# Kernel optimization log

Measured on AMD Instinct MI355X. Metric: run time of the kernel, lower is better.

## Reference

```python
import jax, jax.numpy as jnp
import numpy as np

VAR0, VAR1 = 0.1, 0.2          # SSD encode variances
POS_T, NEG_T, NPR = 0.5, 0.4, 3  # pos/neg thresholds, negpos_ratio
BBOX_ALPHA, CONF_ALPHA = 1.5, 1.0


def point_form(b):
    # cxcywh -> x1y1x2y2
    return jnp.concatenate([b[..., :2] - b[..., 2:] / 2, b[..., :2] + b[..., 2:] / 2], -1)


def jaccard(a, b):
    # a:[n,4], b:[m,4] in xyxy -> IoU [n,m]
    tl = jnp.maximum(a[:, None, :2], b[None, :, :2])
    br = jnp.minimum(a[:, None, 2:], b[None, :, 2:])
    inter = jnp.prod(jnp.clip(br - tl, 0.0), -1)
    area_a = jnp.prod(a[:, 2:] - a[:, :2], -1)[:, None]
    area_b = jnp.prod(b[:, 2:] - b[:, :2], -1)[None, :]
    return inter / jnp.clip(area_a + area_b - inter, 1e-10)


def encode(matched, priors):
    # matched: xyxy GT per prior; priors: cxcywh
    g_c = ((matched[:, :2] + matched[:, 2:]) / 2 - priors[:, :2]) / (VAR0 * priors[:, 2:])
    g_wh = jnp.log(jnp.clip((matched[:, 2:] - matched[:, :2]) / priors[:, 2:], 1e-8)) / VAR1
    return jnp.concatenate([g_c, g_wh], -1)


def match_one(gt_box, gt_lab, priors):
    # gt_box:[G,4] xyxy, gt_lab:[G], priors:[P,4] cxcywh
    ov = jaccard(gt_box, point_form(priors))            # [G,P]
    bt_over = ov.max(0)                                  # best GT overlap per prior [P]
    bt_idx = ov.argmax(0)                                # [P]
    bp_idx = ov.argmax(1)                                # best prior per GT [G]
    G = gt_box.shape[0]
    bt_over = bt_over.at[bp_idx].set(2.0)                # force-match best priors
    bt_idx = bt_idx.at[bp_idx].set(jnp.arange(G))
    matched = gt_box[bt_idx]                             # [P,4]
    conf_t = gt_lab[bt_idx]
    conf_t = jnp.where(bt_over < POS_T, jnp.where(bt_over < NEG_T, 0, -1), conf_t)
    return encode(matched, priors), conf_t


def reference(loc_data, conf_data, priors, gt_bboxes, gt_labels):
    B, P, C = conf_data.shape
    loc_t, conf_t = jax.vmap(match_one)(gt_bboxes, gt_labels, priors)
    loc_t = jax.lax.stop_gradient(loc_t)                 # targets are detached in torch
    pos = conf_t > 0                                     # [B,P]
    num_pos = pos.sum(-1)                                # [B]
    dt = loc_data.dtype
    pos_w = pos.astype(dt) / jnp.clip(num_pos, 1).astype(dt)[:, None]

    # localization: per-image-normalized smooth L1 over positives
    d = loc_data - loc_t
    sl1 = jnp.where(jnp.abs(d) < 1.0, 0.5 * d * d, jnp.abs(d) - 0.5)
    loss_B = (pos_w[:, :, None] * sl1).sum() * BBOX_ALPHA

    # OHEM confidence loss: mine top negpos_ratio*num_pos hardest negatives per image
    loss_c = jax.nn.logsumexp(conf_data, -1) - conf_data[..., 0]
    loss_c = jnp.where(pos | (conf_t < 0), 0.0, jax.lax.stop_gradient(loss_c))
    rank = jnp.argsort(jnp.argsort(-loss_c, -1), -1)     # descending rank [B,P]
    num_neg = jnp.clip(NPR * num_pos, 0, P - 1)
    neg = (rank < num_neg[:, None]) & (conf_t == 0)
    keep = (pos | neg).astype(dt)
    logp = jax.nn.log_softmax(conf_data, -1)
    tgt = jnp.clip(conf_t, 0)
    ce = -jnp.take_along_axis(logp, tgt[..., None], -1)[..., 0]
    loss_C = (keep * ce).sum() * CONF_ALPHA

    return jnp.stack([loss_B, loss_C]) / B               # [2]: (loss_B, loss_C)


def setup_inputs() -> dict:
    key = jax.random.key(0)
    k = jax.random.split(key, 8)
    B, P, C, G = 16, 19248, 81, 16
    loc_data = jax.random.normal(k[0], (B, P, 4), jnp.float32)
    conf_data = jax.random.normal(k[1], (B, P, C), jnp.float32)
    pc = jax.random.uniform(k[2], (B, P, 2)) * 0.9 + 0.05
    pwh = jax.random.uniform(k[3], (B, P, 2)) * 0.25 + 0.05
    priors = jnp.concatenate([pc, pwh], -1).astype(jnp.float32)  # cxcywh
    gc = jax.random.uniform(k[4], (B, G, 2)) * 0.8 + 0.1
    gwh = jax.random.uniform(k[5], (B, G, 2)) * 0.3 + 0.05
    gt_bboxes = jnp.clip(point_form(jnp.concatenate([gc, gwh], -1)), 0.0, 1.0).astype(jnp.float32)
    gt_labels = jax.random.randint(k[6], (B, G), 1, C)
    return {"loc_data": loc_data, "conf_data": conf_data, "priors": priors,
            "gt_bboxes": gt_bboxes, "gt_labels": gt_labels}
```

## Files before the change

### kernel.cpp

```cpp
#include <hip/hip_runtime.h>
#include <math.h>

#define NB 16
#define NP 19248
#define NC 81
#define NG 16
#define NBLK 76
#define NBC 301
#define NWPB (NBC * 4)

static __device__ __forceinline__ float smoothl1(float d) {
    float a = fabsf(d);
    return (a < 1.f) ? 0.5f * d * d : (a - 0.5f);
}

static __device__ __forceinline__ unsigned long long umax64(unsigned long long a, unsigned long long b) {
    return a > b ? a : b;
}

__global__ void k_init(unsigned int* w, float* out) {
    if (threadIdx.x < 512) w[threadIdx.x] = 0u;
    if (threadIdx.x < 2) out[threadIdx.x] = 0.f;
}

__global__ void k_match(const float* __restrict__ priors,
                        const float* __restrict__ gtb,
                        float* __restrict__ bt_over, int* __restrict__ bt_idx,
                        unsigned long long* __restrict__ bp_key) {
    const int b = blockIdx.y;
    const int p = blockIdx.x * 256 + threadIdx.x;
    const bool valid = p < NP;
    __shared__ float4 sgt[NG];
    __shared__ unsigned long long smax[NG];
    if (threadIdx.x < NG) {
        const float* g4 = gtb + (size_t)(b * NG + threadIdx.x) * 4;
        sgt[threadIdx.x] = make_float4(g4[0], g4[1], g4[2], g4[3]);
        smax[threadIdx.x] = 0ULL;
    }
    __syncthreads();
    float4 pr = make_float4(0.f, 0.f, 0.f, 0.f);
    if (valid) pr = *(const float4*)(priors + ((size_t)b * NP + p) * 4);
    float px1 = pr.x - pr.z * 0.5f, py1 = pr.y - pr.w * 0.5f;
    float px2 = pr.x + pr.z * 0.5f, py2 = pr.y + pr.w * 0.5f;
    float areaP = (px2 - px1) * (py2 - py1);
    float best = -1.f; int bi = 0;
    unsigned int pk = 0xFFFFFFFFu - (unsigned int)p;
    #pragma unroll
    for (int g = 0; g < NG; ++g) {
        float4 gb = sgt[g];
        float iw = fminf(gb.z, px2) - fmaxf(gb.x, px1);
        float ih = fminf(gb.w, py2) - fmaxf(gb.y, py1);
        float inter = fmaxf(iw, 0.f) * fmaxf(ih, 0.f);
        float areaG = (gb.z - gb.x) * (gb.w - gb.y);
        float ov = inter / fmaxf(areaG + areaP - inter, 1e-10f);
        if (ov > best) { best = ov; bi = g; }
        unsigned long long key = ((unsigned long long)__float_as_uint(ov) << 32) | pk;
        #pragma unroll
        for (int off = 1; off <= 8; off <<= 1)
            key = umax64(key, (unsigned long long)__shfl_xor((unsigned long long)key, off));
        if ((threadIdx.x & 15) == 0) atomicMax(&smax[g], key);
    }
    if (valid) {
        bt_over[(size_t)b * NP + p] = best;
        bt_idx[(size_t)b * NP + p] = bi;
    }
    __syncthreads();
    if (threadIdx.x < NG) atomicMax(&bp_key[b * NG + threadIdx.x], smax[threadIdx.x]);
}

__global__ void __launch_bounds__(256, 6) k_conf(
        const float* __restrict__ conf,
        const float* __restrict__ loc,
        const float* __restrict__ priors,
        const float* __restrict__ gtb,
        const int* __restrict__ gtl,
        const float* __restrict__ bt_over,
        const int* __restrict__ bt_idx,
        const unsigned long long* __restrict__ bp_key,
        float* __restrict__ mlc,
        int* __restrict__ pnp, float* __restrict__ psl, float* __restrict__ pce) {
    __shared__ float sc[4][1296];
    const int b = blockIdx.y;
    const int tid = threadIdx.x;
    const int w = tid >> 6, lane = tid & 63;
    const int rb = blockIdx.x * 64 + w * 16;
    const bool wvalid = rb < NP;
    const int rb_c = wvalid ? rb : (NP - 16);

    const float4* src = (const float4*)(conf + ((size_t)b * NP + rb_c) * 81);
    float4* dst = (float4*)sc[w];
    #pragma unroll
    for (int i = 0; i < 5; ++i) dst[lane + 64 * i] = src[lane + 64 * i];
    if (lane < 4) dst[lane + 320] = src[lane + 320];
    __builtin_amdgcn_wave_barrier();

    const int r = lane >> 2, c = lane & 3;
    const int p = rb_c + r;
    const int bp = b * NP + p;

    const float over = bt_over[bp];
    int bi = bt_idx[bp];
    int ct;
    if (over < 0.4f) ct = 0;
    else if (over < 0.5f) ct = -1;
    else ct = gtl[b * NG + bi];
    #pragma unroll
    for (int g = NG - 1; g >= 0; --g) {
        unsigned int fp = 0xFFFFFFFFu - (unsigned int)(bp_key[b * NG + g] & 0xFFFFFFFFULL);
        if (fp == (unsigned int)p) { bi = g; ct = gtl[b * NG + g]; break; }
    }
    if (!wvalid) ct = 0;
    const int tgt = ct > 0 ? ct : 0;

    const float* row = sc[w] + r * 81;
    float s = 0.f, ctg = 0.f;
    #pragma unroll
    for (int k = 0; k < 21; ++k) {
        int cc = c + 4 * k;
        if (cc < 81) {
            float v = row[cc];
            s += __expf(v);
            ctg += (cc == tgt) ? v : 0.f;
        }
    }
    s += __shfl_xor(s, 1, 4);   s += __shfl_xor(s, 2, 4);
    ctg += __shfl_xor(ctg, 1, 4); ctg += __shfl_xor(ctg, 2, 4);
    const float c0 = row[0];
    const float lse = __logf(s);

    if (c == 0 && wvalid) mlc[bp] = (ct == 0) ? (lse - c0) : -1.0f;

    float vsl = 0.f, vce = 0.f; int vnp = 0;
    if (c == 0 && ct > 0) {
        const float4 prr = *(const float4*)(priors + (size_t)bp * 4);
        const float* gb = gtb + (size_t)(b * NG + bi) * 4;
        float lt0 = ((gb[0] + gb[2]) * 0.5f - prr.x) / (0.1f * prr.z);
        float lt1 = ((gb[1] + gb[3]) * 0.5f - prr.y) / (0.1f * prr.w);
        float lt2 = logf(fmaxf((gb[2] - gb[0]) / prr.z, 1e-8f)) / 0.2f;
        float lt3 = logf(fmaxf((gb[3] - gb[1]) / prr.w, 1e-8f)) / 0.2f;
        const float4 l4 = *(const float4*)(loc + (size_t)bp * 4);
        vsl = smoothl1(l4.x - lt0) + smoothl1(l4.y - lt1) +
              smoothl1(l4.z - lt2) + smoothl1(l4.w - lt3);
        vce = lse - ctg;
        vnp = 1;
    }
    #pragma unroll
    for (int o = 32; o >= 1; o >>= 1) {
        vnp += __shfl_xor(vnp, o);
        vsl += __shfl_xor(vsl, o);
        vce += __shfl_xor(vce, o);
    }
    if (lane == 0) {
        const int idx = b * NWPB + blockIdx.x * 4 + w;
        pnp[idx] = vnp; psl[idx] = vsl; pce[idx] = vce;
    }
}

__global__ void __launch_bounds__(1024) k_selneg(
        const float* __restrict__ mlc,
        const int* __restrict__ pnp,
        const float* __restrict__ psl,
        const float* __restrict__ pce,
        float* __restrict__ out) {
    const int b = blockIdx.x, tid = threadIdx.x;
    __shared__ unsigned int hist[4096];
    __shared__ unsigned long long list[1024];
    __shared__ unsigned int s_jstar, s_need, s_cnt;
    __shared__ unsigned long long s_thr;
    __shared__ unsigned int wtot[16], wsuf[16];
    __shared__ float wsum[16];
    __shared__ int wnp[16]; __shared__ float wsl[16], wcp[16];
    __shared__ int s_np; __shared__ float s_sl, s_cp;

    const float4* v4 = (const float4*)(mlc + (size_t)b * NP);
    float4 rv[5];
    #pragma unroll
    for (int j = 0; j < 5; ++j) {
        int i = tid + 1024 * j;
        rv[j] = (i < NP / 4) ? v4[i] : make_float4(-1.f, -1.f, -1.f, -1.f);
    }

    {
        int np_ = 0; float sl_ = 0.f, cp_ = 0.f;
        for (int i = tid; i < NWPB; i += 1024) {
            np_ += pnp[b * NWPB + i];
            sl_ += psl[b * NWPB + i];
            cp_ += pce[b * NWPB + i];
        }
        #pragma unroll
        for (int o = 32; o >= 1; o >>= 1) {
            np_ += __shfl_xor(np_, o);
            sl_ += __shfl_xor(sl_, o);
            cp_ += __shfl_xor(cp_, o);
        }
        if ((tid & 63) == 0) { wnp[tid >> 6] = np_; wsl[tid >> 6] = sl_; wcp[tid >> 6] = cp_; }
    }
    if (tid == 0) { s_cnt = 0u; s_thr = ~0ULL; }
    for (int i = tid; i < 4096; i += 1024) hist[i] = 0u;
    __syncthreads();
    if (tid == 0) {
        int np_ = 0; float sl_ = 0.f, cp_ = 0.f;
        #pragma unroll
        for (int i = 0; i < 16; ++i) { np_ += wnp[i]; sl_ += wsl[i]; cp_ += wcp[i]; }
        s_np = np_; s_sl = sl_; s_cp = cp_;
    }
    #pragma unroll
    for (int j = 0; j < 5; ++j) {
        float vv[4] = {rv[j].x, rv[j].y, rv[j].z, rv[j].w};
        #pragma unroll
        for (int c = 0; c < 4; ++c)
            if (vv[c] >= 0.f)
                atomicAdd(&hist[min((unsigned int)(vv[c] * 256.f), 4095u)], 1u);
    }
    __syncthreads();
    const int np = s_np;
    const unsigned int k = (unsigned int)min(3 * np, NP - 1);

    if (k > 0) {
        unsigned int c0 = hist[tid * 4], c1 = hist[tid * 4 + 1],
                     c2 = hist[tid * 4 + 2], c3 = hist[tid * 4 + 3];
        unsigned int t2 = c2 + c3, t1 = c1 + t2, t0 = c0 + t1;
        unsigned int s = t0;
        const int lane = tid & 63, w = tid >> 6;
        #pragma unroll
        for (int o = 1; o < 64; o <<= 1) {
            unsigned int vv = __shfl_down(s, o);
            if (lane + o < 64) s += vv;
        }
        if (lane == 0) wtot[w] = s;
        __syncthreads();
        if (tid < 16) {
            unsigned int acc = 0;
            for (int j = tid + 1; j < 16; ++j) acc += wtot[j];
            wsuf[tid] = acc;
        }
        __syncthreads();
        const unsigned int base = wsuf[w] + (s - t0);
        unsigned int b0 = base + t0, b1 = base + t1, b2 = base + t2, b3 = base + c3;
        hist[tid * 4] = b0; hist[tid * 4 + 1] = b1;
        hist[tid * 4 + 2] = b2; hist[tid * 4 + 3] = b3;
        __syncthreads();
        const unsigned int total = hist[0];
        if (k >= total) {
            if (tid == 0) s_thr = 0ULL;
        } else {
            unsigned int n3 = (tid * 4 + 4 < 4096) ? hist[tid * 4 + 4] : 0u;
            if (b0 >= k && b1 < k) { s_jstar = tid * 4;     s_need = k - b1; }
            if (b1 >= k && b2 < k) { s_jstar = tid * 4 + 1; s_need = k - b2; }
            if (b2 >= k && b3 < k) { s_jstar = tid * 4 + 2; s_need = k - b3; }
            if (b3 >= k && n3 < k) { s_jstar = tid * 4 + 3; s_need = k - n3; }
            __syncthreads();
            const unsigned int jstar = s_jstar, need = s_need;
            #pragma unroll
            for (int j = 0; j < 5; ++j) {
                float vv[4] = {rv[j].x, rv[j].y, rv[j].z, rv[j].w};
                #pragma unroll
                for (int c = 0; c < 4; ++c) {
                    if (vv[c] >= 0.f &&
                        min((unsigned int)(vv[c] * 256.f), 4095u) == jstar) {
                        unsigned int pos = atomicAdd(&s_cnt, 1u);
                        if (pos < 1024u) {
                            int pidx = 4 * (tid + 1024 * j) + c;
                            list[pos] = ((unsigned long long)__float_as_uint(vv[c]) << 32) |
                                        (unsigned long long)(0xFFFFFFFFu - (unsigned int)pidx);
                        }
                    }
                }
            }
            __syncthreads();
            const unsigned int cnt = s_cnt;
            if (cnt <= 1024u) {
                if (tid < (int)cnt) {
                    unsigned long long me = list[tid];
                    unsigned int rk = 0;
                    for (unsigned int j = 0; j < cnt; ++j) rk += (list[j] > me) ? 1u : 0u;
                    if (rk == need - 1) s_thr = me;
                }
            } else if (tid == 0) {
                s_thr = ((unsigned long long)__float_as_uint((float)jstar / 256.f)) << 32;
            }
        }
    }
    __syncthreads();
    const unsigned long long thr = s_thr;

    float sum = 0.f;
    #pragma unroll
    for (int j = 0; j < 5; ++j) {
        float vv[4] = {rv[j].x, rv[j].y, rv[j].z, rv[j].w};
        #pragma unroll
        for (int c = 0; c < 4; ++c) {
            if (vv[c] >= 0.f) {
                int pidx = 4 * (tid + 1024 * j) + c;
                unsigned long long key = ((unsigned long long)__float_as_uint(vv[c]) << 32) |
                                         (unsigned long long)(0xFFFFFFFFu - (unsigned int)pidx);
                if (key >= thr) sum += vv[c];
            }
        }
    }
    #pragma unroll
    for (int o = 32; o >= 1; o >>= 1) sum += __shfl_xor(sum, o);
    if ((tid & 63) == 0) wsum[tid >> 6] = sum;
    __syncthreads();
    if (tid == 0) {
        float neg = 0.f;
        #pragma unroll
        for (int i = 0; i < 16; ++i) neg += wsum[i];
        float lb = s_sl / (float)max(np, 1);
        float lc = s_cp + neg;
        atomicAdd(&out[0], lb * 1.5f / (float)NB);
        atomicAdd(&out[1], lc / (float)NB);
    }
}

extern "C" void kernel_launch(void* const* d_in, const int* in_sizes, int n_in,
                              void* d_out, int out_size, void* d_ws, size_t ws_size,
                              hipStream_t stream) {
    const float* loc    = (const float*)d_in[0];
    const float* conf   = (const float*)d_in[1];
    const float* priors = (const float*)d_in[2];
    const float* gtb    = (const float*)d_in[3];
    const int*   gtl    = (const int*)d_in[4];
    float* out = (float*)d_out;

    char* w = (char*)d_ws;
    const size_t BP4 = (size_t)NB * NP * 4;
    const size_t P1  = (size_t)NB * NWPB * 4;
    unsigned long long* bp_key = (unsigned long long*)w;
    int*   pnp = (int*)  (w + 4096);
    float* psl = (float*)(w + 4096 + P1);
    float* pce = (float*)(w + 4096 + 2 * P1);
    float* bt_over  = (float*)(w + 262144);
    int*   bt_idx   = (int*)  (w + 262144 + BP4);
    float* mlc      = (float*)(w + 262144 + 2 * BP4);

    k_init<<<1, 512, 0, stream>>>((unsigned int*)w, out);
    k_match<<<dim3(NBLK, NB), 256, 0, stream>>>(priors, gtb, bt_over, bt_idx, bp_key);
    k_conf<<<dim3(NBC, NB), 256, 0, stream>>>(conf, loc, priors, gtb, gtl,
                                              bt_over, bt_idx, bp_key, mlc,
                                              pnp, psl, pce);
    k_selneg<<<NB, 1024, 0, stream>>>(mlc, pnp, psl, pce, out);
}
```

Measured before the change: 188.0 us.

## Recompute per-prior best-GT overlap in conf kernel instead of storing it

```diff
diff --git a/kernel.cpp b/kernel.cpp
--- a/kernel.cpp
+++ b/kernel.cpp
@@ -5,7 +5,7 @@
 #define NP 19248
 #define NC 81
 #define NG 16
-#define NBLK 76
+#define NBM 19
 #define NBC 301
 #define NWPB (NBC * 4)
 
@@ -25,11 +25,8 @@
 
 __global__ void k_match(const float* __restrict__ priors,
                         const float* __restrict__ gtb,
-                        float* __restrict__ bt_over, int* __restrict__ bt_idx,
                         unsigned long long* __restrict__ bp_key) {
     const int b = blockIdx.y;
-    const int p = blockIdx.x * 256 + threadIdx.x;
-    const bool valid = p < NP;
     __shared__ float4 sgt[NG];
     __shared__ unsigned long long smax[NG];
     if (threadIdx.x < NG) {
@@ -38,44 +35,48 @@
         smax[threadIdx.x] = 0ULL;
     }
     __syncthreads();
-    float4 pr = make_float4(0.f, 0.f, 0.f, 0.f);
-    if (valid) pr = *(const float4*)(priors + ((size_t)b * NP + p) * 4);
-    float px1 = pr.x - pr.z * 0.5f, py1 = pr.y - pr.w * 0.5f;
-    float px2 = pr.x + pr.z * 0.5f, py2 = pr.y + pr.w * 0.5f;
-    float areaP = (px2 - px1) * (py2 - py1);
-    float best = -1.f; int bi = 0;
-    unsigned int pk = 0xFFFFFFFFu - (unsigned int)p;
+    unsigned long long kb[NG];
+    #pragma unroll
+    for (int g = 0; g < NG; ++g) kb[g] = 0ULL;
+    #pragma unroll
+    for (int i = 0; i < 4; ++i) {
+        const int p = blockIdx.x * 1024 + i * 256 + threadIdx.x;
+        const bool valid = p < NP;
+        float4 pr = make_float4(0.f, 0.f, 0.f, 0.f);
+        if (valid) pr = *(const float4*)(priors + ((size_t)b * NP + p) * 4);
+        float px1 = pr.x - pr.z * 0.5f, py1 = pr.y - pr.w * 0.5f;
+        float px2 = pr.x + pr.z * 0.5f, py2 = pr.y + pr.w * 0.5f;
+        float areaP = (px2 - px1) * (py2 - py1);
+        unsigned int pk = 0xFFFFFFFFu - (unsigned int)p;
+        #pragma unroll
+        for (int g = 0; g < NG; ++g) {
+            float4 gb = sgt[g];
+            float iw = fminf(gb.z, px2) - fmaxf(gb.x, px1);
+            float ih = fminf(gb.w, py2) - fmaxf(gb.y, py1);
+            float inter = fmaxf(iw, 0.f) * fmaxf(ih, 0.f);
+            float areaG = (gb.z - gb.x) * (gb.w - gb.y);
+            float ov = inter / fmaxf(areaG + areaP - inter, 1e-10f);
+            kb[g] = umax64(kb[g], ((unsigned long long)__float_as_uint(ov) << 32) | pk);
+        }
+    }
     #pragma unroll
     for (int g = 0; g < NG; ++g) {
-        float4 gb = sgt[g];
-        float iw = fminf(gb.z, px2) - fmaxf(gb.x, px1);
-        float ih = fminf(gb.w, py2) - fmaxf(gb.y, py1);
-        float inter = fmaxf(iw, 0.f) * fmaxf(ih, 0.f);
-        float areaG = (gb.z - gb.x) * (gb.w - gb.y);
-        float ov = inter / fmaxf(areaG + areaP - inter, 1e-10f);
-        if (ov > best) { best = ov; bi = g; }
-        unsigned long long key = ((unsigned long long)__float_as_uint(ov) << 32) | pk;
+        unsigned long long key = kb[g];
         #pragma unroll
         for (int off = 1; off <= 8; off <<= 1)
             key = umax64(key, (unsigned long long)__shfl_xor((unsigned long long)key, off));
         if ((threadIdx.x & 15) == 0) atomicMax(&smax[g], key);
     }
-    if (valid) {
-        bt_over[(size_t)b * NP + p] = best;
-        bt_idx[(size_t)b * NP + p] = bi;
-    }
     __syncthreads();
     if (threadIdx.x < NG) atomicMax(&bp_key[b * NG + threadIdx.x], smax[threadIdx.x]);
 }
 
-__global__ void __launch_bounds__(256, 6) k_conf(
+__global__ void __launch_bounds__(256, 4) k_conf(
         const float* __restrict__ conf,
         const float* __restrict__ loc,
         const float* __restrict__ priors,
         const float* __restrict__ gtb,
         const int* __restrict__ gtl,
-        const float* __restrict__ bt_over,
-        const int* __restrict__ bt_idx,
         const unsigned long long* __restrict__ bp_key,
         float* __restrict__ mlc,
         int* __restrict__ pnp, float* __restrict__ psl, float* __restrict__ pce) {
@@ -92,14 +93,34 @@
     #pragma unroll
     for (int i = 0; i < 5; ++i) dst[lane + 64 * i] = src[lane + 64 * i];
     if (lane < 4) dst[lane + 320] = src[lane + 320];
-    __builtin_amdgcn_wave_barrier();
 
     const int r = lane >> 2, c = lane & 3;
     const int p = rb_c + r;
     const int bp = b * NP + p;
 
-    const float over = bt_over[bp];
-    int bi = bt_idx[bp];
+    const float4 prr = *(const float4*)(priors + (size_t)bp * 4);
+    const float px1 = prr.x - prr.z * 0.5f, py1 = prr.y - prr.w * 0.5f;
+    const float px2 = prr.x + prr.z * 0.5f, py2 = prr.y + prr.w * 0.5f;
+    const float areaP = (px2 - px1) * (py2 - py1);
+    unsigned long long kq = 0ULL;
+    #pragma unroll
+    for (int j = 0; j < 4; ++j) {
+        const int g = c * 4 + j;
+        const float* g4 = gtb + (size_t)(b * NG + g) * 4;
+        float gx1 = g4[0], gy1 = g4[1], gx2 = g4[2], gy2 = g4[3];
+        float iw = fminf(gx2, px2) - fmaxf(gx1, px1);
+        float ih = fminf(gy2, py2) - fmaxf(gy1, py1);
+        float inter = fmaxf(iw, 0.f) * fmaxf(ih, 0.f);
+        float areaG = (gx2 - gx1) * (gy2 - gy1);
+        float ov = inter / fmaxf(areaG + areaP - inter, 1e-10f);
+        kq = umax64(kq, ((unsigned long long)__float_as_uint(ov) << 32) |
+                        (unsigned long long)(15 - g));
+    }
+    kq = umax64(kq, (unsigned long long)__shfl_xor((unsigned long long)kq, 1, 4));
+    kq = umax64(kq, (unsigned long long)__shfl_xor((unsigned long long)kq, 2, 4));
+    const float over = __uint_as_float((unsigned int)(kq >> 32));
+    int bi = 15 - (int)(kq & 0xFULL);
+
     int ct;
     if (over < 0.4f) ct = 0;
     else if (over < 0.5f) ct = -1;
@@ -111,6 +132,8 @@
     }
     if (!wvalid) ct = 0;
     const int tgt = ct > 0 ? ct : 0;
+
+    __builtin_amdgcn_wave_barrier();
 
     const float* row = sc[w] + r * 81;
     float s = 0.f, ctg = 0.f;
@@ -132,7 +155,6 @@
 
     float vsl = 0.f, vce = 0.f; int vnp = 0;
     if (c == 0 && ct > 0) {
-        const float4 prr = *(const float4*)(priors + (size_t)bp * 4);
         const float* gb = gtb + (size_t)(b * NG + bi) * 4;
         float lt0 = ((gb[0] + gb[2]) * 0.5f - prr.x) / (0.1f * prr.z);
         float lt1 = ((gb[1] + gb[3]) * 0.5f - prr.y) / (0.1f * prr.w);
@@ -324,20 +346,16 @@
     float* out = (float*)d_out;
 
     char* w = (char*)d_ws;
-    const size_t BP4 = (size_t)NB * NP * 4;
-    const size_t P1  = (size_t)NB * NWPB * 4;
+    const size_t P1 = (size_t)NB * NWPB * 4;
     unsigned long long* bp_key = (unsigned long long*)w;
     int*   pnp = (int*)  (w + 4096);
     float* psl = (float*)(w + 4096 + P1);
     float* pce = (float*)(w + 4096 + 2 * P1);
-    float* bt_over  = (float*)(w + 262144);
-    int*   bt_idx   = (int*)  (w + 262144 + BP4);
-    float* mlc      = (float*)(w + 262144 + 2 * BP4);
+    float* mlc = (float*)(w + 262144);
 
     k_init<<<1, 512, 0, stream>>>((unsigned int*)w, out);
-    k_match<<<dim3(NBLK, NB), 256, 0, stream>>>(priors, gtb, bt_over, bt_idx, bp_key);
+    k_match<<<dim3(NBM, NB), 256, 0, stream>>>(priors, gtb, bp_key);
     k_conf<<<dim3(NBC, NB), 256, 0, stream>>>(conf, loc, priors, gtb, gtl,
-                                              bt_over, bt_idx, bp_key, mlc,
-                                              pnp, psl, pce);
+                                              bp_key, mlc, pnp, psl, pce);
     k_selneg<<<NB, 1024, 0, stream>>>(mlc, pnp, psl, pce, out);
 }
```

Measured after the change: 213.7 us. 13.7% more time.
